# Kernel tuning notes

Measured on AMD Instinct MI355X. Metric: run time of the kernel, lower is better.

The kernel has to match this reference:

```python
import jax, jax.numpy as jnp
import numpy as np

N = 131072   # total atoms in flat batch
E = 262144   # total bonds (directed edges)
G = 4096     # number of molecules (graphs)
FN = 30      # atom feature dim
FE = 11      # bond feature dim
H = 256      # hidden_dim
L = 5        # num GINE layers
BN_EPS = 1e-5


def _bn(x, g, b, m, v):
    # BatchNorm1d in eval mode: affine with running stats
    return g * (x - m) * jax.lax.rsqrt(v + BN_EPS) + b


def setup_inputs() -> dict:
    key = jax.random.key(0)
    ks = jax.random.split(key, 48)
    s = 0.05  # weight scale to keep 5-layer residual stack well-conditioned
    inp = {
        'x': jax.random.normal(ks[0], (N, FN), jnp.float32),
        'edge_index': jax.random.randint(ks[1], (2, E), 0, N),
        'batch': jnp.sort(jax.random.randint(ks[2], (N,), 0, G)),
        'edge_attr': jax.random.normal(ks[3], (E, FE), jnp.float32),
        # encoders
        'enc_w': s * jax.random.normal(ks[4], (FN, H), jnp.float32),
        'enc_b': jnp.zeros((H,), jnp.float32),
        'bond_w': s * jax.random.normal(ks[5], (FE, H), jnp.float32),
        'bond_b': jnp.zeros((H,), jnp.float32),
        # per-layer GINE params (stacked over L)
        'eps': jnp.zeros((L,), jnp.float32),
        'w1': s * jax.random.normal(ks[6], (L, H, 2 * H), jnp.float32),
        'b1': jnp.zeros((L, 2 * H), jnp.float32),
        'ibn_g': 1.0 + 0.1 * jax.random.normal(ks[7], (L, 2 * H), jnp.float32),
        'ibn_b': 0.1 * jax.random.normal(ks[8], (L, 2 * H), jnp.float32),
        'ibn_m': 0.1 * jax.random.normal(ks[9], (L, 2 * H), jnp.float32),
        'ibn_v': jnp.ones((L, 2 * H), jnp.float32),
        'w2': s * jax.random.normal(ks[10], (L, 2 * H, H), jnp.float32),
        'b2': jnp.zeros((L, H), jnp.float32),
        'obn_g': 1.0 + 0.1 * jax.random.normal(ks[11], (L, H), jnp.float32),
        'obn_b': 0.1 * jax.random.normal(ks[12], (L, H), jnp.float32),
        'obn_m': 0.1 * jax.random.normal(ks[13], (L, H), jnp.float32),
        'obn_v': jnp.ones((L, H), jnp.float32),
        # classifier
        'cw1': s * jax.random.normal(ks[14], (2 * H, H), jnp.float32),
        'cb1': jnp.zeros((H,), jnp.float32),
        'c1g': 1.0 + 0.1 * jax.random.normal(ks[15], (H,), jnp.float32),
        'c1b': 0.1 * jax.random.normal(ks[16], (H,), jnp.float32),
        'c1m': 0.1 * jax.random.normal(ks[17], (H,), jnp.float32),
        'c1v': jnp.ones((H,), jnp.float32),
        'cw2': s * jax.random.normal(ks[18], (H, H // 2), jnp.float32),
        'cb2': jnp.zeros((H // 2,), jnp.float32),
        'c2g': 1.0 + 0.1 * jax.random.normal(ks[19], (H // 2,), jnp.float32),
        'c2b': 0.1 * jax.random.normal(ks[20], (H // 2,), jnp.float32),
        'c2m': 0.1 * jax.random.normal(ks[21], (H // 2,), jnp.float32),
        'c2v': jnp.ones((H // 2,), jnp.float32),
        'cw3': s * jax.random.normal(ks[22], (H // 2, 1), jnp.float32),
        'cb3': jnp.zeros((1,), jnp.float32),
    }
    return inp


def reference(x, edge_index, batch, edge_attr,
              enc_w, enc_b, bond_w, bond_b,
              eps, w1, b1, ibn_g, ibn_b, ibn_m, ibn_v,
              w2, b2, obn_g, obn_b, obn_m, obn_v,
              cw1, cb1, c1g, c1b, c1m, c1v,
              cw2, cb2, c2g, c2b, c2m, c2v,
              cw3, cb3):
    n = x.shape[0]
    src, dst = edge_index[0], edge_index[1]
    h = x @ enc_w + enc_b                      # [N, H]
    e = edge_attr @ bond_w + bond_b           # [E, H]
    for i in range(L):
        h_in = h
        # GINEConv: (1+eps)*x_i + sum_j relu(x_j + e_ji), then MLP
        msg = jax.nn.relu(h[src] + e)                          # [E, H] gather
        agg = jax.ops.segment_sum(msg, dst, num_segments=n)    # [N, H] scatter-add
        z = (1.0 + eps[i]) * h + agg
        z = jax.nn.relu(_bn(z @ w1[i] + b1[i], ibn_g[i], ibn_b[i], ibn_m[i], ibn_v[i]))
        z = z @ w2[i] + b2[i]
        # outer BN + relu (dropout is identity in eval) + residual
        h = jax.nn.relu(_bn(z, obn_g[i], obn_b[i], obn_m[i], obn_v[i])) + h_in
    # global mean + max pooling by graph id
    counts = jax.ops.segment_sum(jnp.ones((n,), h.dtype), batch, num_segments=G)
    sums = jax.ops.segment_sum(h, batch, num_segments=G)
    mean_p = sums / jnp.maximum(counts, 1.0)[:, None]
    max_p = jax.ops.segment_max(h, batch, num_segments=G)
    max_p = jnp.where(counts[:, None] > 0, max_p, 0.0)
    p = jnp.concatenate([mean_p, max_p], axis=1)               # [G, 2H]
    # classifier (eval mode: dropout off, BN uses running stats)
    q = jax.nn.relu(_bn(p @ cw1 + cb1, c1g, c1b, c1m, c1v))
    q = jax.nn.relu(_bn(q @ cw2 + cb2, c2g, c2b, c2m, c2v))
    out = q @ cw3 + cb3
    return out[:, 0]                                           # [G]
```

## Files before the change

### kernel.cpp

```cpp
#include <hip/hip_runtime.h>
#include <math.h>

#define NA 131072
#define NE 262144
#define NG 4096
#define FN 30
#define FE 11
#define H  256
#define H2 512
#define NL 5
#define BN_EPS 1e-5f
#define KP 32

typedef _Float16 f16x8 __attribute__((ext_vector_type(8)));
typedef _Float16 f16x4 __attribute__((ext_vector_type(4)));
typedef float f32x4 __attribute__((ext_vector_type(4)));

static char* g_buf = nullptr;
__attribute__((constructor)) static void _alloc_private_ws() {
    void* p = nullptr;
    if (hipMalloc(&p, (size_t)320 * 1024 * 1024) == hipSuccess) g_buf = (char*)p;
}

__global__ __launch_bounds__(256) void prep_w_all(const float* __restrict__ w, int K, int N,
                                                  _Float16* __restrict__ hT) {
    const float* wl = w + (size_t)blockIdx.z * K * N;
    _Float16* hTl = hT + (size_t)blockIdx.z * K * N;
    __shared__ float t[32][33];
    const int k0 = blockIdx.x * 32, n0 = blockIdx.y * 32;
    const int tx = threadIdx.x & 31, ty = threadIdx.x >> 5;
    #pragma unroll
    for (int i = 0; i < 4; ++i)
        t[ty + i * 8][tx] = wl[(size_t)(k0 + ty + i * 8) * N + n0 + tx];
    __syncthreads();
    #pragma unroll
    for (int i = 0; i < 4; ++i)
        hTl[(size_t)(n0 + ty + i * 8) * K + k0 + tx] = (_Float16)t[tx][ty + i * 8];
}

__global__ __launch_bounds__(256) void prep_wpad(const float* __restrict__ w, int K_IN,
                                                 _Float16* __restrict__ wT) {
    const int n = threadIdx.x;
    #pragma unroll
    for (int kk = 0; kk < KP / 8; ++kk) {
        f16x8 v;
        #pragma unroll
        for (int j = 0; j < 8; ++j) {
            const int k = kk * 8 + j;
            v[j] = (k < K_IN) ? (_Float16)w[(size_t)k * H + n] : (_Float16)0.0f;
        }
        *(f16x8*)(wT + (size_t)n * KP + kk * 8) = v;
    }
}

__global__ __launch_bounds__(256) void prep_x16(const float* __restrict__ x,
                                                _Float16* __restrict__ x16) {
    const int row = blockIdx.x * 64 + (threadIdx.x >> 2);
    const int g = threadIdx.x & 3;
    f16x8 v;
    #pragma unroll
    for (int j = 0; j < 8; ++j) {
        const int c = g * 8 + j;
        v[j] = (c < FN) ? (_Float16)x[(size_t)row * FN + c] : (_Float16)0.0f;
    }
    *(f16x8*)(x16 + (size_t)row * KP + g * 8) = v;
}

__global__ __launch_bounds__(256) void prep_ea16(const float* __restrict__ eattr,
                                                 const int2* __restrict__ se,
                                                 _Float16* __restrict__ ea16) {
    const int t = blockIdx.x * 64 + (threadIdx.x >> 2);
    const int g = threadIdx.x & 3;
    const int e = se[t].y;
    f16x8 v;
    #pragma unroll
    for (int j = 0; j < 8; ++j) {
        const int c = g * 8 + j;
        v[j] = (c < FE) ? (_Float16)eattr[(size_t)e * FE + c] : (_Float16)0.0f;
    }
    *(f16x8*)(ea16 + (size_t)t * KP + g * 8) = v;
}

__global__ __launch_bounds__(256) void count_deg(const int* __restrict__ ei,
                                                 int* __restrict__ deg) {
    const int e = blockIdx.x * 256 + threadIdx.x;
    if (e < NE) atomicAdd(&deg[ei[NE + e]], 1);
}

__global__ __launch_bounds__(1024) void scan_deg(const int* __restrict__ deg,
                                                 int* __restrict__ rowptr,
                                                 int* __restrict__ cursor) {
    __shared__ int part[1024];
    const int t = threadIdx.x;
    const int base = t * 128;
    int s = 0;
    #pragma unroll 8
    for (int i = 0; i < 128; ++i) s += deg[base + i];
    part[t] = s;
    __syncthreads();
    for (int off = 1; off < 1024; off <<= 1) {
        const int v = (t >= off) ? part[t - off] : 0;
        __syncthreads();
        part[t] += v;
        __syncthreads();
    }
    int run = (t == 0) ? 0 : part[t - 1];
    #pragma unroll 8
    for (int i = 0; i < 128; ++i) {
        rowptr[base + i] = run;
        cursor[base + i] = run;
        run += deg[base + i];
    }
    if (t == 1023) rowptr[NA] = run;
}

__global__ __launch_bounds__(256) void fill_elist(const int* __restrict__ ei,
                                                  int* __restrict__ cursor,
                                                  int2* __restrict__ se) {
    const int e = blockIdx.x * 256 + threadIdx.x;
    if (e < NE) {
        const int src = ei[e];
        const int pos = atomicAdd(&cursor[ei[NE + e]], 1);
        se[pos] = make_int2(src, e);
    }
}

__global__ __launch_bounds__(256) void gine_msg(const _Float16* __restrict__ h16,
                                                const _Float16* __restrict__ eb,
                                                const int2* __restrict__ se,
                                                const int* __restrict__ rowptr,
                                                const float* __restrict__ eps, int l,
                                                _Float16* __restrict__ z) {
    const int dst = blockIdx.x * 4 + (threadIdx.x >> 6);
    const int lane = threadIdx.x & 63;
    const int c = lane * 4;
    const float sc = 1.0f + eps[l];
    const f16x4 hv = *(const f16x4*)(h16 + (size_t)dst * H + c);
    float4 acc;
    acc.x = sc * (float)hv.x; acc.y = sc * (float)hv.y;
    acc.z = sc * (float)hv.z; acc.w = sc * (float)hv.w;
    const int lo = rowptr[dst], hi = rowptr[dst + 1];
    for (int t = lo; t < hi; ++t) {
        const int src = se[t].x;
        const f16x4 hs = *(const f16x4*)(h16 + (size_t)src * H + c);
        const f16x4 ev = *(const f16x4*)(eb + (size_t)t * H + c);
        acc.x += fmaxf((float)hs.x + (float)ev.x, 0.0f);
        acc.y += fmaxf((float)hs.y + (float)ev.y, 0.0f);
        acc.z += fmaxf((float)hs.z + (float)ev.z, 0.0f);
        acc.w += fmaxf((float)hs.w + (float)ev.w, 0.0f);
    }
    f16x4 o;
    o.x = (_Float16)acc.x; o.y = (_Float16)acc.y;
    o.z = (_Float16)acc.z; o.w = (_Float16)acc.w;
    *(f16x4*)(z + (size_t)dst * H + c) = o;
}

__global__ __launch_bounds__(512, 4) void fused_mlp(
    const _Float16* __restrict__ Az,
    const _Float16* __restrict__ W1T,
    const _Float16* __restrict__ W2T,
    const float* __restrict__ b1l, const float* __restrict__ ig,
    const float* __restrict__ ib, const float* __restrict__ im,
    const float* __restrict__ iv,
    const float* __restrict__ b2l, const float* __restrict__ og,
    const float* __restrict__ ob, const float* __restrict__ om,
    const float* __restrict__ ov,
    _Float16* __restrict__ Hio)
{
    __shared__ f16x8 Bs[1024];
    __shared__ _Float16 Z1[64 * 512];

    const int tid = threadIdx.x;
    const int m0 = blockIdx.x * 64;
    const int lane = tid & 63, wv = tid >> 6;
    const int lrow = lane & 15, lgrp = lane >> 4;
    const int wm2 = wv >> 2, wn2 = wv & 3;
    const int kq = tid & 3;
    const int brow = tid >> 2;
    const int bsw0 = brow * 4 + (kq ^ ((brow >> 1) & 3));
    const int bsw1 = (brow + 128) * 4 + (kq ^ (((brow + 128) >> 1) & 3));

    const int ar0 = m0 + wm2 * 32 + lrow;
    const int ar1 = ar0 + 16;

    f16x8 bA, bB;
    #define SLOAD_B(BASE, K0, KD) { \
        bA = *(const f16x8*)((BASE) + (size_t)brow * (KD) + (K0) + kq * 8); \
        bB = *(const f16x8*)((BASE) + (size_t)(brow + 128) * (KD) + (K0) + kq * 8); }
    #define SWRITE_B() { Bs[bsw0] = bA; Bs[bsw1] = bB; }

    const f32x4 zero4 = {0.0f, 0.0f, 0.0f, 0.0f};

    #pragma unroll 1
    for (int h = 0; h < 2; ++h) {
        const _Float16* Bb = W1T + (size_t)h * 256 * 256;
        float scl1[4], shf1[4];
        #pragma unroll
        for (int ni = 0; ni < 4; ++ni) {
            const int c = h * 256 + wn2 * 64 + ni * 16 + lrow;
            const float s = ig[c] * rsqrtf(iv[c] + BN_EPS);
            scl1[ni] = s;
            shf1[ni] = s * (b1l[c] - im[c]) + ib[c];
        }
        f32x4 acc[2][4];
        #pragma unroll
        for (int i = 0; i < 2; ++i)
            #pragma unroll
            for (int j = 0; j < 4; ++j) acc[i][j] = zero4;

        f16x8 a0c = *(const f16x8*)(Az + (size_t)ar0 * 256 + lgrp * 8);
        f16x8 a1c = *(const f16x8*)(Az + (size_t)ar1 * 256 + lgrp * 8);
        SLOAD_B(Bb, 0, 256);
        #pragma unroll 1
        for (int ks = 0; ks < 8; ++ks) {
            __syncthreads();
            SWRITE_B();
            __syncthreads();
            f16x8 a0n, a1n;
            if (ks + 1 < 8) {
                SLOAD_B(Bb, (ks + 1) * 32, 256);
                a0n = *(const f16x8*)(Az + (size_t)ar0 * 256 + (ks + 1) * 32 + lgrp * 8);
                a1n = *(const f16x8*)(Az + (size_t)ar1 * 256 + (ks + 1) * 32 + lgrp * 8);
            }
            f16x8 bf[4];
            #pragma unroll
            for (int ni = 0; ni < 4; ++ni) {
                const int br = wn2 * 64 + ni * 16 + lrow;
                bf[ni] = Bs[br * 4 + (lgrp ^ ((br >> 1) & 3))];
            }
            #pragma unroll
            for (int ni = 0; ni < 4; ++ni) {
                acc[0][ni] = __builtin_amdgcn_mfma_f32_16x16x32_f16(a0c, bf[ni], acc[0][ni], 0, 0, 0);
                acc[1][ni] = __builtin_amdgcn_mfma_f32_16x16x32_f16(a1c, bf[ni], acc[1][ni], 0, 0, 0);
            }
            a0c = a0n; a1c = a1n;
        }
        #pragma unroll
        for (int mi = 0; mi < 2; ++mi)
            #pragma unroll
            for (int j = 0; j < 4; ++j) {
                const int row = wm2 * 32 + mi * 16 + lgrp * 4 + j;
                #pragma unroll
                for (int ni = 0; ni < 4; ++ni) {
                    const int col = h * 256 + wn2 * 64 + ni * 16 + lrow;
                    const int slot = (col >> 3) ^ (row & 7);
                    Z1[row * 512 + (slot << 3) + (col & 7)] =
                        (_Float16)fmaxf(scl1[ni] * acc[mi][ni][j] + shf1[ni], 0.0f);
                }
            }
    }

    float scl2[4], shf2[4];
    #pragma unroll
    for (int ni = 0; ni < 4; ++ni) {
        const int c = wn2 * 64 + ni * 16 + lrow;
        const float s = og[c] * rsqrtf(ov[c] + BN_EPS);
        scl2[ni] = s;
        shf2[ni] = s * (b2l[c] - om[c]) + ob[c];
    }
    f32x4 acc2[2][4];
    #pragma unroll
    for (int i = 0; i < 2; ++i)
        #pragma unroll
        for (int j = 0; j < 4; ++j) acc2[i][j] = zero4;

    SLOAD_B(W2T, 0, 512);
    #pragma unroll 1
    for (int ks = 0; ks < 16; ++ks) {
        __syncthreads();
        SWRITE_B();
        __syncthreads();
        if (ks + 1 < 16) SLOAD_B(W2T, (ks + 1) * 32, 512);
        const int k0 = ks * 32;
        f16x8 af[2], bf[4];
        #pragma unroll
        for (int mi = 0; mi < 2; ++mi) {
            const int ar = wm2 * 32 + mi * 16 + lrow;
            const int slot = ((k0 >> 3) + lgrp) ^ (ar & 7);
            af[mi] = *(const f16x8*)&Z1[ar * 512 + (slot << 3)];
        }
        #pragma unroll
        for (int ni = 0; ni < 4; ++ni) {
            const int br = wn2 * 64 + ni * 16 + lrow;
            bf[ni] = Bs[br * 4 + (lgrp ^ ((br >> 1) & 3))];
        }
        #pragma unroll
        for (int mi = 0; mi < 2; ++mi)
            #pragma unroll
            for (int ni = 0; ni < 4; ++ni)
                acc2[mi][ni] = __builtin_amdgcn_mfma_f32_16x16x32_f16(af[mi], bf[ni], acc2[mi][ni], 0, 0, 0);
    }
    #pragma unroll
    for (int mi = 0; mi < 2; ++mi)
        #pragma unroll
        for (int j = 0; j < 4; ++j) {
            const int row = m0 + wm2 * 32 + mi * 16 + lgrp * 4 + j;
            #pragma unroll
            for (int ni = 0; ni < 4; ++ni) {
                const int col = wn2 * 64 + ni * 16 + lrow;
                float v = fmaxf(scl2[ni] * acc2[mi][ni][j] + shf2[ni], 0.0f);
                v += (float)Hio[(size_t)row * H + col];
                Hio[(size_t)row * H + col] = (_Float16)v;
            }
        }
    #undef SLOAD_B
    #undef SWRITE_B
}

template <int KDIM, int EPI>
__global__ __launch_bounds__(256, 4) void gemm_f16(
    const _Float16* __restrict__ A,
    const _Float16* __restrict__ BT,
    int Ncols,
    const float* __restrict__ bias, const float* __restrict__ bng,
    const float* __restrict__ bnb, const float* __restrict__ bnm,
    const float* __restrict__ bnv,
    _Float16* __restrict__ C16, const _Float16* __restrict__ res)
{
    __shared__ f16x8 As[2][512];
    __shared__ f16x8 Bs[2][512];

    const int tid = threadIdx.x;
    const int nt = Ncols >> 7;
    const int nwg = gridDim.x, orig = blockIdx.x;
    const int q = nwg >> 3, r = nwg & 7;
    const int xcd = orig & 7, rk = orig >> 3;
    const int wg = (xcd < r ? xcd * (q + 1) : r * (q + 1) + (xcd - r) * q) + rk;
    const int m0 = (wg / nt) * 128;
    const int n0 = (wg % nt) * 128;

    const int wid = tid >> 6, lane = tid & 63;
    const int wm = wid >> 1, wn = wid & 1;
    const int lrow = lane & 15, lgrp = lane >> 4;
    const int r0s = tid >> 2;
    const int kq  = tid & 3;
    const int sw0 = kq ^ ((r0s >> 1) & 3);
    const int sw1 = kq ^ (((r0s + 64) >> 1) & 3);

    f32x4 acc[4][4];
    const f32x4 zero4 = {0.0f, 0.0f, 0.0f, 0.0f};
    #pragma unroll
    for (int i = 0; i < 4; ++i)
        #pragma unroll
        for (int j = 0; j < 4; ++j) acc[i][j] = zero4;

    f16x8 a0, a1, b0, b1;
    #define SLOAD(K0)                                                             \
        a0 = *(const f16x8*)(A  + (size_t)(m0 + r0s) * KDIM + (K0) + kq * 8);     \
        a1 = *(const f16x8*)(A  + (size_t)(m0 + r0s + 64) * KDIM + (K0) + kq * 8);\
        b0 = *(const f16x8*)(BT + (size_t)(n0 + r0s) * KDIM + (K0) + kq * 8);     \
        b1 = *(const f16x8*)(BT + (size_t)(n0 + r0s + 64) * KDIM + (K0) + kq * 8);
    #define SWRITE(CUR)                                                           \
        As[CUR][r0s * 4 + sw0] = a0;  As[CUR][(r0s + 64) * 4 + sw1] = a1;         \
        Bs[CUR][r0s * 4 + sw0] = b0;  Bs[CUR][(r0s + 64) * 4 + sw1] = b1;

    SLOAD(0);
    int cur = 0;
    for (int k0 = 0; k0 < KDIM; k0 += 32) {
        SWRITE(cur);
        __syncthreads();
        if (k0 + 32 < KDIM) { SLOAD(k0 + 32); }
        f16x8 af[4], bf[4];
        #pragma unroll
        for (int mi = 0; mi < 4; ++mi) {
            const int ar = wm * 64 + mi * 16 + lrow;
            af[mi] = As[cur][ar * 4 + (lgrp ^ ((ar >> 1) & 3))];
        }
        #pragma unroll
        for (int ni = 0; ni < 4; ++ni) {
            const int br = wn * 64 + ni * 16 + lrow;
            bf[ni] = Bs[cur][br * 4 + (lgrp ^ ((br >> 1) & 3))];
        }
        #pragma unroll
        for (int mi = 0; mi < 4; ++mi)
            #pragma unroll
            for (int ni = 0; ni < 4; ++ni)
                acc[mi][ni] = __builtin_amdgcn_mfma_f32_16x16x32_f16(af[mi], bf[ni], acc[mi][ni], 0, 0, 0);
        cur ^= 1;
    }
    #undef SLOAD
    #undef SWRITE

    float scl[4], shf[4];
    #pragma unroll
    for (int ni = 0; ni < 4; ++ni) {
        const int c = n0 + wn * 64 + ni * 16 + lrow;
        if (EPI == 2) {
            scl[ni] = 1.0f;
            shf[ni] = bias[c];
        } else {
            const float s = bng[c] * rsqrtf(bnv[c] + BN_EPS);
            scl[ni] = s;
            shf[ni] = s * (bias[c] - bnm[c]) + bnb[c];
        }
    }
    #pragma unroll
    for (int mi = 0; mi < 4; ++mi)
        #pragma unroll
        for (int j = 0; j < 4; ++j) {
            const int row = m0 + wm * 64 + mi * 16 + lgrp * 4 + j;
            #pragma unroll
            for (int ni = 0; ni < 4; ++ni) {
                const int col = n0 + wn * 64 + ni * 16 + lrow;
                float v = scl[ni] * acc[mi][ni][j] + shf[ni];
                if (EPI != 2) v = fmaxf(v, 0.0f);
                C16[(size_t)row * Ncols + col] = (_Float16)v;
            }
        }
}

__global__ __launch_bounds__(H) void pool_kernel(const _Float16* __restrict__ h16,
                                                 const int* __restrict__ batch,
                                                 _Float16* __restrict__ p16) {
    const int g = blockIdx.x;
    const int c = threadIdx.x;
    int lo, hi;
    {
        int a = 0, b = NA;
        while (a < b) { int mid = (a + b) >> 1; if (batch[mid] < g) a = mid + 1; else b = mid; }
        lo = a;
        b = NA;
        while (a < b) { int mid = (a + b) >> 1; if (batch[mid] < g + 1) a = mid + 1; else b = mid; }
        hi = a;
    }
    float sum = 0.0f, mx = -INFINITY;
    for (int n = lo; n < hi; ++n) {
        const float v = (float)h16[(size_t)n * H + c];
        sum += v;
        mx = fmaxf(mx, v);
    }
    const int cnt = hi - lo;
    const float mean = (cnt > 0) ? sum / (float)cnt : 0.0f;
    if (cnt == 0) mx = 0.0f;
    p16[(size_t)g * H2 + c] = (_Float16)mean;
    p16[(size_t)g * H2 + H + c] = (_Float16)mx;
}

__global__ __launch_bounds__(64) void final_out(const _Float16* __restrict__ q2,
                                                const float* __restrict__ w,
                                                const float* __restrict__ b,
                                                float* __restrict__ out) {
    const int g = blockIdx.x;
    const int lane = threadIdx.x;
    float acc = (float)q2[(size_t)g * 128 + lane] * w[lane]
              + (float)q2[(size_t)g * 128 + 64 + lane] * w[64 + lane];
    #pragma unroll
    for (int off = 32; off > 0; off >>= 1) acc += __shfl_down(acc, off);
    if (lane == 0) out[g] = acc + b[0];
}

extern "C" void kernel_launch(void* const* d_in, const int* in_sizes, int n_in,
                              void* d_out, int out_size, void* d_ws, size_t ws_size,
                              hipStream_t stream) {
    const float* x      = (const float*)d_in[0];
    const int*   ei     = (const int*)d_in[1];
    const int*   batch  = (const int*)d_in[2];
    const float* eattr  = (const float*)d_in[3];
    const float* enc_w  = (const float*)d_in[4];
    const float* enc_b  = (const float*)d_in[5];
    const float* bond_w = (const float*)d_in[6];
    const float* bond_b = (const float*)d_in[7];
    const float* eps    = (const float*)d_in[8];
    const float* w1     = (const float*)d_in[9];
    const float* b1     = (const float*)d_in[10];
    const float* ibn_g  = (const float*)d_in[11];
    const float* ibn_b  = (const float*)d_in[12];
    const float* ibn_m  = (const float*)d_in[13];
    const float* ibn_v  = (const float*)d_in[14];
    const float* w2     = (const float*)d_in[15];
    const float* b2     = (const float*)d_in[16];
    const float* obn_g  = (const float*)d_in[17];
    const float* obn_b  = (const float*)d_in[18];
    const float* obn_m  = (const float*)d_in[19];
    const float* obn_v  = (const float*)d_in[20];
    const float* cw1    = (const float*)d_in[21];
    const float* cb1    = (const float*)d_in[22];
    const float* c1g    = (const float*)d_in[23];
    const float* c1b    = (const float*)d_in[24];
    const float* c1m    = (const float*)d_in[25];
    const float* c1v    = (const float*)d_in[26];
    const float* cw2    = (const float*)d_in[27];
    const float* cb2    = (const float*)d_in[28];
    const float* c2g    = (const float*)d_in[29];
    const float* c2b    = (const float*)d_in[30];
    const float* c2m    = (const float*)d_in[31];
    const float* c2v    = (const float*)d_in[32];
    const float* cw3    = (const float*)d_in[33];
    const float* cb3    = (const float*)d_in[34];
    float* out = (float*)d_out;

    const size_t WTE       = (size_t)NL * H * H2;
    const size_t CW1E      = (size_t)H2 * H;
    const size_t CW2E      = (size_t)H * (H / 2);
    const size_t EWE       = (size_t)H * KP;
    const size_t BWE       = (size_t)H * KP;
    const size_t wt_bytes  = (2 * WTE + CW1E + CW2E + EWE + BWE) * 2;
    const size_t csr_words = (size_t)3 * NA + 1 + 2 * (size_t)NE + 63;
    const size_t csr_bytes = csr_words * 4;
    const size_t eb_bytes  = (size_t)NE * H * 2;
    const size_t h16_bytes = (size_t)NA * H * 2;
    const size_t z_bytes   = (size_t)NA * H * 2;
    const size_t x16_bytes = (size_t)NA * KP * 2;
    const size_t ea_bytes  = (size_t)NE * KP * 2;
    const size_t need_full = wt_bytes + csr_bytes + eb_bytes + h16_bytes + z_bytes
                           + x16_bytes + ea_bytes;

    char* buf;
    if (ws_size >= need_full) { buf = (char*)d_ws; }
    else if (g_buf)           { buf = g_buf; }
    else                      { buf = (char*)d_ws; }

    _Float16* w1T  = (_Float16*)buf;
    _Float16* w2T  = w1T + WTE;
    _Float16* cw1T = w2T + WTE;
    _Float16* cw2T = cw1T + CW1E;
    _Float16* encT = cw2T + CW2E;
    _Float16* bndT = encT + EWE;
    int*  deg    = (int*)(buf + wt_bytes);
    int*  rowptr = deg + NA;
    int*  cursor = rowptr + NA + 1;
    int2* se     = (int2*)(cursor + NA);
    _Float16* eb  = (_Float16*)(buf + wt_bytes + csr_bytes);
    _Float16* h16 = (_Float16*)((char*)eb + eb_bytes);
    _Float16* z   = (_Float16*)((char*)h16 + h16_bytes);
    _Float16* x16  = (_Float16*)((char*)z + z_bytes);
    _Float16* ea16 = (_Float16*)((char*)x16 + x16_bytes);

    _Float16* p16 = z;
    _Float16* q1  = p16 + (size_t)NG * H2;
    _Float16* q2  = q1 + (size_t)NG * H;

    prep_w_all<<<dim3(H / 32, H2 / 32, NL), 256, 0, stream>>>(w1, H, H2, w1T);
    prep_w_all<<<dim3(H2 / 32, H / 32, NL), 256, 0, stream>>>(w2, H2, H, w2T);
    prep_w_all<<<dim3(H2 / 32, H / 32, 1), 256, 0, stream>>>(cw1, H2, H, cw1T);
    prep_w_all<<<dim3(H / 32, H / 64, 1), 256, 0, stream>>>(cw2, H, H / 2, cw2T);
    prep_wpad<<<1, 256, 0, stream>>>(enc_w, FN, encT);
    prep_wpad<<<1, 256, 0, stream>>>(bond_w, FE, bndT);

    hipMemsetAsync(deg, 0, (size_t)NA * 4, stream);
    count_deg<<<NE / 256, 256, 0, stream>>>(ei, deg);
    scan_deg<<<1, 1024, 0, stream>>>(deg, rowptr, cursor);
    fill_elist<<<NE / 256, 256, 0, stream>>>(ei, cursor, se);

    prep_x16<<<NA / 64, 256, 0, stream>>>(x, x16);
    prep_ea16<<<NE / 64, 256, 0, stream>>>(eattr, se, ea16);

    gemm_f16<KP, 2><<<(NA / 128) * (H / 128), 256, 0, stream>>>(
        x16, encT, H, enc_b, nullptr, nullptr, nullptr, nullptr, h16, nullptr);
    gemm_f16<KP, 2><<<(NE / 128) * (H / 128), 256, 0, stream>>>(
        ea16, bndT, H, bond_b, nullptr, nullptr, nullptr, nullptr, eb, nullptr);

    for (int l = 0; l < NL; ++l) {
        gine_msg<<<NA / 4, 256, 0, stream>>>(h16, eb, se, rowptr, eps, l, z);
        fused_mlp<<<NA / 64, 512, 0, stream>>>(
            z, w1T + (size_t)l * H * H2, w2T + (size_t)l * H2 * H,
            b1 + (size_t)l * H2, ibn_g + (size_t)l * H2, ibn_b + (size_t)l * H2,
            ibn_m + (size_t)l * H2, ibn_v + (size_t)l * H2,
            b2 + (size_t)l * H, obn_g + (size_t)l * H, obn_b + (size_t)l * H,
            obn_m + (size_t)l * H, obn_v + (size_t)l * H,
            h16);
    }

    pool_kernel<<<NG, H, 0, stream>>>(h16, batch, p16);
    gemm_f16<H2, 0><<<(NG / 128) * (H / 128), 256, 0, stream>>>(
        p16, cw1T, H, cb1, c1g, c1b, c1m, c1v, q1, nullptr);
    gemm_f16<H, 0><<<(NG / 128) * ((H / 2) / 128), 256, 0, stream>>>(
        q1, cw2T, H / 2, cb2, c2g, c2b, c2m, c2v, q2, nullptr);
    final_out<<<NG, 64, 0, stream>>>(q2, cw3, cb3, out);
}
```

Baseline: 1.282 ms.

## Double-buffer weight tiles in fused MLP and merge first GEMM halves

```diff
diff --git a/kernel.cpp b/kernel.cpp
--- a/kernel.cpp
+++ b/kernel.cpp
@@ -155,7 +155,7 @@
     *(f16x4*)(z + (size_t)dst * H + c) = o;
 }
 
-__global__ __launch_bounds__(512, 4) void fused_mlp(
+__global__ __launch_bounds__(512, 2) void fused_mlp(
     const _Float16* __restrict__ Az,
     const _Float16* __restrict__ W1T,
     const _Float16* __restrict__ W2T,
@@ -167,7 +167,7 @@
     const float* __restrict__ ov,
     _Float16* __restrict__ Hio)
 {
-    __shared__ f16x8 Bs[1024];
+    __shared__ f16x8 BsRaw[4096];
     __shared__ _Float16 Z1[64 * 512];
 
     const int tid = threadIdx.x;
@@ -177,72 +177,79 @@
     const int wm2 = wv >> 2, wn2 = wv & 3;
     const int kq = tid & 3;
     const int brow = tid >> 2;
-    const int bsw0 = brow * 4 + (kq ^ ((brow >> 1) & 3));
-    const int bsw1 = (brow + 128) * 4 + (kq ^ (((brow + 128) >> 1) & 3));
 
     const int ar0 = m0 + wm2 * 32 + lrow;
     const int ar1 = ar0 + 16;
 
-    f16x8 bA, bB;
-    #define SLOAD_B(BASE, K0, KD) { \
-        bA = *(const f16x8*)((BASE) + (size_t)brow * (KD) + (K0) + kq * 8); \
-        bB = *(const f16x8*)((BASE) + (size_t)(brow + 128) * (KD) + (K0) + kq * 8); }
-    #define SWRITE_B() { Bs[bsw0] = bA; Bs[bsw1] = bB; }
-
     const f32x4 zero4 = {0.0f, 0.0f, 0.0f, 0.0f};
 
-    #pragma unroll 1
-    for (int h = 0; h < 2; ++h) {
-        const _Float16* Bb = W1T + (size_t)h * 256 * 256;
-        float scl1[4], shf1[4];
-        #pragma unroll
-        for (int ni = 0; ni < 4; ++ni) {
-            const int c = h * 256 + wn2 * 64 + ni * 16 + lrow;
+    {
+        float scl1[8], shf1[8];
+        #pragma unroll
+        for (int ni = 0; ni < 8; ++ni) {
+            const int c = wn2 * 128 + ni * 16 + lrow;
             const float s = ig[c] * rsqrtf(iv[c] + BN_EPS);
             scl1[ni] = s;
             shf1[ni] = s * (b1l[c] - im[c]) + ib[c];
         }
-        f32x4 acc[2][4];
+        f32x4 acc[2][8];
         #pragma unroll
         for (int i = 0; i < 2; ++i)
             #pragma unroll
-            for (int j = 0; j < 4; ++j) acc[i][j] = zero4;
+            for (int j = 0; j < 8; ++j) acc[i][j] = zero4;
+
+        f16x8 bR[4];
+        #define SLOAD_B4(K0) { \
+            bR[0] = *(const f16x8*)(W1T + (size_t)(brow      ) * 256 + (K0) + kq * 8); \
+            bR[1] = *(const f16x8*)(W1T + (size_t)(brow + 128) * 256 + (K0) + kq * 8); \
+            bR[2] = *(const f16x8*)(W1T + (size_t)(brow + 256) * 256 + (K0) + kq * 8); \
+            bR[3] = *(const f16x8*)(W1T + (size_t)(brow + 384) * 256 + (K0) + kq * 8); }
+        #define SWRITE_B4(CUR) { \
+            f16x8* bp = &BsRaw[(CUR) * 2048]; \
+            bp[(brow      ) * 4 + (kq ^ (((brow      ) >> 1) & 3))] = bR[0]; \
+            bp[(brow + 128) * 4 + (kq ^ (((brow + 128) >> 1) & 3))] = bR[1]; \
+            bp[(brow + 256) * 4 + (kq ^ (((brow + 256) >> 1) & 3))] = bR[2]; \
+            bp[(brow + 384) * 4 + (kq ^ (((brow + 384) >> 1) & 3))] = bR[3]; }
 
         f16x8 a0c = *(const f16x8*)(Az + (size_t)ar0 * 256 + lgrp * 8);
         f16x8 a1c = *(const f16x8*)(Az + (size_t)ar1 * 256 + lgrp * 8);
-        SLOAD_B(Bb, 0, 256);
+        SLOAD_B4(0);
+        int cur = 0;
         #pragma unroll 1
         for (int ks = 0; ks < 8; ++ks) {
-            __syncthreads();
-            SWRITE_B();
+            SWRITE_B4(cur);
             __syncthreads();
             f16x8 a0n, a1n;
             if (ks + 1 < 8) {
-                SLOAD_B(Bb, (ks + 1) * 32, 256);
+                SLOAD_B4((ks + 1) * 32);
                 a0n = *(const f16x8*)(Az + (size_t)ar0 * 256 + (ks + 1) * 32 + lgrp * 8);
                 a1n = *(const f16x8*)(Az + (size_t)ar1 * 256 + (ks + 1) * 32 + lgrp * 8);
             }
-            f16x8 bf[4];
-            #pragma unroll
-            for (int ni = 0; ni < 4; ++ni) {
-                const int br = wn2 * 64 + ni * 16 + lrow;
-                bf[ni] = Bs[br * 4 + (lgrp ^ ((br >> 1) & 3))];
+            const f16x8* bp = &BsRaw[cur * 2048];
+            f16x8 bf[8];
+            #pragma unroll
+            for (int ni = 0; ni < 8; ++ni) {
+                const int br = wn2 * 128 + ni * 16 + lrow;
+                bf[ni] = bp[br * 4 + (lgrp ^ ((br >> 1) & 3))];
             }
             #pragma unroll
-            for (int ni = 0; ni < 4; ++ni) {
+            for (int ni = 0; ni < 8; ++ni) {
                 acc[0][ni] = __builtin_amdgcn_mfma_f32_16x16x32_f16(a0c, bf[ni], acc[0][ni], 0, 0, 0);
                 acc[1][ni] = __builtin_amdgcn_mfma_f32_16x16x32_f16(a1c, bf[ni], acc[1][ni], 0, 0, 0);
             }
-            a0c = a0n; a1c = a1n;
-        }
+            a0c = a0n; a1c = a1n; cur ^= 1;
+        }
+        #undef SLOAD_B4
+        #undef SWRITE_B4
+
         #pragma unroll
         for (int mi = 0; mi < 2; ++mi)
             #pragma unroll
             for (int j = 0; j < 4; ++j) {
                 const int row = wm2 * 32 + mi * 16 + lgrp * 4 + j;
                 #pragma unroll
-                for (int ni = 0; ni < 4; ++ni) {
-                    const int col = h * 256 + wn2 * 64 + ni * 16 + lrow;
+                for (int ni = 0; ni < 8; ++ni) {
+                    const int col = wn2 * 128 + ni * 16 + lrow;
                     const int slot = (col >> 3) ^ (row & 7);
                     Z1[row * 512 + (slot << 3) + (col & 7)] =
                         (_Float16)fmaxf(scl1[ni] * acc[mi][ni][j] + shf1[ni], 0.0f);
@@ -264,14 +271,25 @@
         #pragma unroll
         for (int j = 0; j < 4; ++j) acc2[i][j] = zero4;
 
-    SLOAD_B(W2T, 0, 512);
+    f16x8 bA, bB;
+    #define SLOAD_B2(K0) { \
+        bA = *(const f16x8*)(W2T + (size_t)brow * 512 + (K0) + kq * 8); \
+        bB = *(const f16x8*)(W2T + (size_t)(brow + 128) * 512 + (K0) + kq * 8); }
+    #define SWRITE_B2(CUR) { \
+        f16x8* bp = &BsRaw[(CUR) * 1024]; \
+        bp[brow * 4 + (kq ^ ((brow >> 1) & 3))] = bA; \
+        bp[(brow + 128) * 4 + (kq ^ (((brow + 128) >> 1) & 3))] = bB; }
+
+    SLOAD_B2(0);
+    __syncthreads();
+    int cur2 = 0;
     #pragma unroll 1
     for (int ks = 0; ks < 16; ++ks) {
+        SWRITE_B2(cur2);
         __syncthreads();
-        SWRITE_B();
-        __syncthreads();
-        if (ks + 1 < 16) SLOAD_B(W2T, (ks + 1) * 32, 512);
+        if (ks + 1 < 16) SLOAD_B2((ks + 1) * 32);
         const int k0 = ks * 32;
+        const f16x8* bp = &BsRaw[cur2 * 1024];
         f16x8 af[2], bf[4];
         #pragma unroll
         for (int mi = 0; mi < 2; ++mi) {
@@ -282,14 +300,18 @@
         #pragma unroll
         for (int ni = 0; ni < 4; ++ni) {
             const int br = wn2 * 64 + ni * 16 + lrow;
-            bf[ni] = Bs[br * 4 + (lgrp ^ ((br >> 1) & 3))];
+            bf[ni] = bp[br * 4 + (lgrp ^ ((br >> 1) & 3))];
         }
         #pragma unroll
         for (int mi = 0; mi < 2; ++mi)
             #pragma unroll
             for (int ni = 0; ni < 4; ++ni)
                 acc2[mi][ni] = __builtin_amdgcn_mfma_f32_16x16x32_f16(af[mi], bf[ni], acc2[mi][ni], 0, 0, 0);
-    }
+        cur2 ^= 1;
+    }
+    #undef SLOAD_B2
+    #undef SWRITE_B2
+
     #pragma unroll
     for (int mi = 0; mi < 2; ++mi)
         #pragma unroll
@@ -303,8 +325,6 @@
                 Hio[(size_t)row * H + col] = (_Float16)v;
             }
         }
-    #undef SLOAD_B
-    #undef SWRITE_B
 }
 
 template <int KDIM, int EPI>
```

New measurement: 1.376 ms. 7.3% more time.
